# Kernel tuning notes

Measured on AMD Instinct MI355X. Metric: run time of the kernel, lower is better.

Reference implementation:

```python
import jax, jax.numpy as jnp
import numpy as np

HEADS = 4
OUT = 64  # hidden_channels


def gat_conv(x, src, dst, N, W, att_src, att_dst, bias):
    # x: [N, Fin] -> h: [N, H, C]
    h = (x @ W).reshape(N, HEADS, OUT)
    a_s = (h * att_src).sum(-1)  # [N, H]
    a_d = (h * att_dst).sum(-1)  # [N, H]
    logits = jax.nn.leaky_relu(a_s[src] + a_d[dst], negative_slope=0.2)  # [E, H]
    # segment softmax over incoming edges of each destination node
    m = jax.ops.segment_max(logits, dst, num_segments=N)
    e = jnp.exp(logits - m[dst])
    z = jax.ops.segment_sum(e, dst, num_segments=N)
    alpha = e / (z[dst] + 1e-16)
    out = jax.ops.segment_sum(h[src] * alpha[:, :, None], dst, num_segments=N)
    return out.reshape(N, HEADS * OUT) + bias


def setup_inputs() -> dict:
    key = jax.random.key(0)
    ks = jax.random.split(key, 16)
    N, E, F = 50000, 800000, 128
    HC = HEADS * OUT  # 256
    s = 0.1
    return {
        "x": jax.random.normal(ks[0], (N, F), jnp.float32),
        "edge_index": jax.random.randint(ks[1], (2, E), 0, N, dtype=jnp.int32),
        "W1": jax.random.normal(ks[2], (F, HC), jnp.float32) * s,
        "as1": jax.random.normal(ks[3], (1, HEADS, OUT), jnp.float32) * s,
        "ad1": jax.random.normal(ks[4], (1, HEADS, OUT), jnp.float32) * s,
        "b1": jnp.zeros((HC,), jnp.float32),
        "W2": jax.random.normal(ks[5], (HC, HC), jnp.float32) * s,
        "as2": jax.random.normal(ks[6], (1, HEADS, OUT), jnp.float32) * s,
        "ad2": jax.random.normal(ks[7], (1, HEADS, OUT), jnp.float32) * s,
        "b2": jnp.zeros((HC,), jnp.float32),
        "lw1": jax.random.normal(ks[8], (HC, OUT), jnp.float32) * s,
        "lb1": jnp.zeros((OUT,), jnp.float32),
        "lw2": jax.random.normal(ks[9], (OUT, 2), jnp.float32) * s,
        "lb2": jnp.zeros((2,), jnp.float32),
    }


def reference(x, edge_index, W1, as1, ad1, b1, W2, as2, ad2, b2, lw1, lb1, lw2, lb2):
    N = x.shape[0]
    # PyG GATConv default add_self_loops=True
    loop = jnp.arange(N, dtype=edge_index.dtype)
    src = jnp.concatenate([edge_index[0], loop])
    dst = jnp.concatenate([edge_index[1], loop])
    h = jax.nn.elu(gat_conv(x, src, dst, N, W1, as1, ad1, b1))
    # dropout is identity at inference
    h = jax.nn.elu(gat_conv(h, src, dst, N, W2, as2, ad2, b2))
    h = jax.nn.relu(h @ lw1 + lb1)
    return jax.nn.log_softmax(h @ lw2 + lb2, axis=1)
```

## Files before the change

kernel.cpp:

```cpp
#include <hip/hip_runtime.h>
#include <math.h>


typedef __attribute__((ext_vector_type(8))) _Float16 half8v;
typedef __attribute__((ext_vector_type(4))) float f32x4;

__device__ __forceinline__ float lrelu(float x) { return x > 0.f ? x : 0.2f * x; }
__device__ __forceinline__ float elu1(float x) { return x > 0.f ? x : (__expf(x) - 1.f); }

__global__ void convert_weights_kernel(const float* __restrict__ W1, const float* __restrict__ W2,
                                       const float* __restrict__ lw1,
                                       _Float16* __restrict__ o1, _Float16* __restrict__ o2,
                                       _Float16* __restrict__ o3, int* __restrict__ indeg,
                                       int N) {
  int t = blockIdx.x * blockDim.x + threadIdx.x;
  if (t < 32768) {
    int n = t >> 7, k = t & 127;
    o1[t] = (_Float16)W1[(long)k * 256 + n];
  } else if (t < 98304) {
    int i = t - 32768;
    int n = i >> 8, k = i & 255;
    o2[i] = (_Float16)W2[(long)k * 256 + n];
  } else if (t < 114688) {
    int i = t - 98304;
    int n = i >> 8, k = i & 255;
    o3[i] = (_Float16)lw1[(long)k * 64 + n];
  } else if (t < 114688 + N) {
    indeg[t - 114688] = 0;
  }
}

__global__ void count_kernel(const int* __restrict__ dst, int E, int* __restrict__ indeg) {
  int e = blockIdx.x * blockDim.x + threadIdx.x;
  if (e < E) atomicAdd(&indeg[dst[e]], 1);
}

__global__ void scan_block_kernel(const int* __restrict__ in, int* __restrict__ incl,
                                  int* __restrict__ bsum, int N) {
  __shared__ int wsum[16];
  int gid = blockIdx.x * 1024 + threadIdx.x;
  int lane = threadIdx.x & 63, w = threadIdx.x >> 6;
  int v = (gid < N) ? in[gid] : 0;
  int sv = v;
#pragma unroll
  for (int o = 1; o < 64; o <<= 1) {
    int t = __shfl_up(sv, o);
    if (lane >= o) sv += t;
  }
  if (lane == 63) wsum[w] = sv;
  __syncthreads();
  if (w == 0) {
    int bs = (lane < 16) ? wsum[lane] : 0;
#pragma unroll
    for (int o = 1; o < 16; o <<= 1) {
      int t = __shfl_up(bs, o);
      if (lane >= o) bs += t;
    }
    if (lane < 16) wsum[lane] = bs;
  }
  __syncthreads();
  if (w > 0) sv += wsum[w - 1];
  if (gid < N) incl[gid] = sv;
  if (threadIdx.x == 1023) bsum[blockIdx.x] = sv;
}

__global__ void scan_finalize_kernel(const int* __restrict__ in, const int* __restrict__ incl,
                                     const int* __restrict__ bsum, int* __restrict__ off,
                                     int* __restrict__ cursor, int N) {
  int gid = blockIdx.x * blockDim.x + threadIdx.x;
  if (gid >= N) return;
  int b = gid >> 10;
  int carry = 0;
  for (int k = 0; k < b; ++k) carry += bsum[k];
  int ic = incl[gid] + carry;
  off[gid + 1] = ic;
  cursor[gid] = ic - in[gid];
  if (gid == 0) off[0] = 0;
}

__global__ void fill_kernel(const int* __restrict__ src, const int* __restrict__ dst, int E,
                            int* __restrict__ cursor, int* __restrict__ csr_src) {
  int e = blockIdx.x * blockDim.x + threadIdx.x;
  if (e < E) {
    int pos = atomicAdd(&cursor[dst[e]], 1);
    csr_src[pos] = src[e];
  }
}

template <typename AT>
__launch_bounds__(256)
__global__ void mfma_gemm_attn_kernel(const AT* __restrict__ A,
                                      const _Float16* __restrict__ B,
                                      const float* __restrict__ att_s,
                                      const float* __restrict__ att_d,
                                      _Float16* __restrict__ C,
                                      float* __restrict__ a_s, float* __restrict__ a_d,
                                      int M, int K) {
  __shared__ _Float16 As[64][40];
  __shared__ _Float16 Bs[2][64][40];
  int tid = threadIdx.x;
  int bm = blockIdx.y * 64, bn = blockIdx.x * 128;
  int lane = tid & 63, wave = tid >> 6;
  int srow = tid >> 2, sch = (tid & 3) * 8;
  const AT* Ap = A + (long)(bm + srow) * K + sch;
  const _Float16* Bp0 = B + (long)(bn + srow) * K + sch;
  const _Float16* Bp1 = B + (long)(bn + 64 + srow) * K + sch;
  bool arow_ok = (bm + srow) < M;
  int fm = lane & 15, fq = lane >> 4;
  f32x4 acc[2][4];
#pragma unroll
  for (int t = 0; t < 2; ++t)
#pragma unroll
    for (int cb = 0; cb < 4; ++cb) acc[t][cb] = (f32x4){0.f, 0.f, 0.f, 0.f};
  for (int k0 = 0; k0 < K; k0 += 32) {
    half8v a8 = {0, 0, 0, 0, 0, 0, 0, 0};
    if (arow_ok) {
      if constexpr (sizeof(AT) == 4) {
        float4 f0 = *(const float4*)(Ap + k0);
        float4 f1 = *(const float4*)(Ap + k0 + 4);
        a8 = (half8v){(_Float16)f0.x, (_Float16)f0.y, (_Float16)f0.z, (_Float16)f0.w,
                      (_Float16)f1.x, (_Float16)f1.y, (_Float16)f1.z, (_Float16)f1.w};
      } else {
        a8 = *(const half8v*)(Ap + k0);
      }
    }
    uint4 vb0 = *(const uint4*)(Bp0 + k0);
    uint4 vb1 = *(const uint4*)(Bp1 + k0);
    *(half8v*)&As[srow][sch] = a8;
    *(uint4*)&Bs[0][srow][sch] = vb0;
    *(uint4*)&Bs[1][srow][sch] = vb1;
    __syncthreads();
    half8v ah = *(const half8v*)&As[wave * 16 + fm][fq * 8];
#pragma unroll
    for (int t = 0; t < 2; ++t)
#pragma unroll
      for (int cb = 0; cb < 4; ++cb) {
        half8v bh = *(const half8v*)&Bs[t][cb * 16 + fm][fq * 8];
        acc[t][cb] = __builtin_amdgcn_mfma_f32_16x16x32_f16(ah, bh, acc[t][cb], 0, 0, 0);
      }
    __syncthreads();
  }
  int row0 = bm + wave * 16 + fq * 4;
#pragma unroll
  for (int t = 0; t < 2; ++t) {
    int headi = blockIdx.x * 2 + t;
    int cbase = bn + t * 64;
    float asv[4], adv[4];
#pragma unroll
    for (int cb = 0; cb < 4; ++cb) {
      int col = cbase + cb * 16 + fm;
      asv[cb] = att_s[col];
      adv[cb] = att_d[col];
    }
#pragma unroll
    for (int r = 0; r < 4; ++r) {
      int row = row0 + r;
      float sp = 0.f, dp = 0.f;
#pragma unroll
      for (int cb = 0; cb < 4; ++cb) {
        float v = acc[t][cb][r];
        sp = fmaf(v, asv[cb], sp);
        dp = fmaf(v, adv[cb], dp);
        if (row < M) C[(long)row * 256 + cbase + cb * 16 + fm] = (_Float16)v;
      }
#pragma unroll
      for (int o = 1; o < 16; o <<= 1) {
        sp += __shfl_xor(sp, o);
        dp += __shfl_xor(dp, o);
      }
      if (fm == 0 && row < M) {
        a_s[(long)row * 4 + headi] = sp;
        a_d[(long)row * 4 + headi] = dp;
      }
    }
  }
}

__launch_bounds__(256)
__global__ void head_mfma_kernel(const _Float16* __restrict__ A, const _Float16* __restrict__ B,
                                 const float* __restrict__ lb1, const float* __restrict__ lw2,
                                 const float* __restrict__ lb2, float* __restrict__ out, int M) {
  __shared__ _Float16 As[64][40];
  __shared__ _Float16 Bs[64][40];
  int tid = threadIdx.x;
  int bm = blockIdx.x * 64;
  int lane = tid & 63, wave = tid >> 6;
  int srow = tid >> 2, sch = (tid & 3) * 8;
  const _Float16* Ap = A + (long)(bm + srow) * 256 + sch;
  const _Float16* Bp = B + (long)srow * 256 + sch;
  int fm = lane & 15, fq = lane >> 4;
  f32x4 acc[4];
#pragma unroll
  for (int cb = 0; cb < 4; ++cb) acc[cb] = (f32x4){0.f, 0.f, 0.f, 0.f};
  for (int k0 = 0; k0 < 256; k0 += 32) {
    uint4 va = *(const uint4*)(Ap + k0);
    uint4 vb = *(const uint4*)(Bp + k0);
    *(uint4*)&As[srow][sch] = va;
    *(uint4*)&Bs[srow][sch] = vb;
    __syncthreads();
    half8v ah = *(const half8v*)&As[wave * 16 + fm][fq * 8];
#pragma unroll
    for (int cb = 0; cb < 4; ++cb) {
      half8v bh = *(const half8v*)&Bs[cb * 16 + fm][fq * 8];
      acc[cb] = __builtin_amdgcn_mfma_f32_16x16x32_f16(ah, bh, acc[cb], 0, 0, 0);
    }
    __syncthreads();
  }
  float lb1c[4], w20[4], w21[4];
#pragma unroll
  for (int cb = 0; cb < 4; ++cb) {
    int col = cb * 16 + fm;
    lb1c[cb] = lb1[col];
    w20[cb] = lw2[col * 2 + 0];
    w21[cb] = lw2[col * 2 + 1];
  }
  float b20 = lb2[0], b21 = lb2[1];
#pragma unroll
  for (int r = 0; r < 4; ++r) {
    float v0 = 0.f, v1 = 0.f;
#pragma unroll
    for (int cb = 0; cb < 4; ++cb) {
      float s = fmaxf(acc[cb][r] + lb1c[cb], 0.f);
      v0 = fmaf(s, w20[cb], v0);
      v1 = fmaf(s, w21[cb], v1);
    }
#pragma unroll
    for (int o = 1; o < 16; o <<= 1) {
      v0 += __shfl_xor(v0, o);
      v1 += __shfl_xor(v1, o);
    }
    if (fm == 0) {
      int row = bm + wave * 16 + fq * 4 + r;
      if (row < M) {
        v0 += b20;
        v1 += b21;
        float mx = fmaxf(v0, v1);
        float ls = mx + logf(expf(v0 - mx) + expf(v1 - mx));
        out[(long)row * 2 + 0] = v0 - ls;
        out[(long)row * 2 + 1] = v1 - ls;
      }
    }
  }
}

__launch_bounds__(256)
__global__ void gat_aggregate8_kernel(const _Float16* __restrict__ h,
                                      const float* __restrict__ a_s,
                                      const float* __restrict__ a_d,
                                      const int* __restrict__ off,
                                      const int* __restrict__ csr_src,
                                      const float* __restrict__ bias,
                                      _Float16* __restrict__ outp, int N) {
  int wid = (blockIdx.x * blockDim.x + threadIdx.x) >> 6;
  int lane = threadIdx.x & 63;
  if (wid >= N) return;
  int c = lane & 31, hlf = lane >> 5, head4 = c >> 3;
  int h1 = lane & 3, sl1 = lane >> 2;
  int beg = off[wid], cnt = off[wid + 1] - beg;
  float ad_h1 = a_d[wid * 4 + h1];
  float m = lrelu(a_s[wid * 4 + h1] + ad_h1);
  float acc[8] = {};
  float z = 0.f;
  if (hlf == 0) {
    z = 1.f;
    half8v sr = *(const half8v*)(h + (long)wid * 256 + c * 8);
#pragma unroll
    for (int i = 0; i < 8; ++i) acc[i] = (float)sr[i];
  }
  for (int c0 = 0; c0 < cnt; c0 += 16) {
    int i2 = c0 + (lane & 15);
    int sv = (i2 < cnt) ? csr_src[beg + i2] : 0;
    int i1 = c0 + sl1;
    int spi = __shfl(sv, sl1);
    float l = (i1 < cnt) ? lrelu(a_s[(long)spi * 4 + h1] + ad_h1) : -1e30f;
    float lm = l;
    lm = fmaxf(lm, __shfl_xor(lm, 4));
    lm = fmaxf(lm, __shfl_xor(lm, 8));
    lm = fmaxf(lm, __shfl_xor(lm, 16));
    lm = fmaxf(lm, __shfl_xor(lm, 32));
    float m_new = fmaxf(m, lm);
    float alpha = __expf(m - m_new);
    float pv = (i1 < cnt) ? __expf(l - m_new) : 0.f;
    m = m_new;
    float alpha4 = __shfl(alpha, head4);
    z *= alpha4;
#pragma unroll
    for (int i = 0; i < 8; ++i) acc[i] *= alpha4;
#pragma unroll 4
    for (int j = 0; j < 16; j += 2) {
      if (c0 + j >= cnt) break;
      int e = j + hlf;
      int s = __shfl(sv, e);
      float p = __shfl(pv, e * 4 + head4);
      z += p;
      half8v rv = *(const half8v*)(h + (long)s * 256 + c * 8);
      acc[0] = fmaf(p, (float)rv[0], acc[0]);
      acc[1] = fmaf(p, (float)rv[1], acc[1]);
      acc[2] = fmaf(p, (float)rv[2], acc[2]);
      acc[3] = fmaf(p, (float)rv[3], acc[3]);
      acc[4] = fmaf(p, (float)rv[4], acc[4]);
      acc[5] = fmaf(p, (float)rv[5], acc[5]);
      acc[6] = fmaf(p, (float)rv[6], acc[6]);
      acc[7] = fmaf(p, (float)rv[7], acc[7]);
    }
  }
  z += __shfl_xor(z, 32);
#pragma unroll
  for (int i = 0; i < 8; ++i) acc[i] += __shfl_xor(acc[i], 32);
  if (hlf == 0) {
    float inv = 1.f / z;
    half8v o;
#pragma unroll
    for (int i = 0; i < 8; ++i) o[i] = (_Float16)elu1(fmaf(acc[i], inv, bias[c * 8 + i]));
    *(half8v*)(outp + (long)wid * 256 + c * 8) = o;
  }
}

static inline int cdiv(int a, int b) { return (a + b - 1) / b; }

extern "C" void kernel_launch(void* const* d_in, const int* in_sizes, int n_in,
                              void* d_out, int out_size, void* d_ws, size_t ws_size,
                              hipStream_t stream) {
  const float* x = (const float*)d_in[0];
  const int* ei = (const int*)d_in[1];
  const float* W1 = (const float*)d_in[2];
  const float* as1 = (const float*)d_in[3];
  const float* ad1 = (const float*)d_in[4];
  const float* b1 = (const float*)d_in[5];
  const float* W2 = (const float*)d_in[6];
  const float* as2 = (const float*)d_in[7];
  const float* ad2 = (const float*)d_in[8];
  const float* b2 = (const float*)d_in[9];
  const float* lw1 = (const float*)d_in[10];
  const float* lb1 = (const float*)d_in[11];
  const float* lw2 = (const float*)d_in[12];
  const float* lb2 = (const float*)d_in[13];
  float* out = (float*)d_out;

  int N = in_sizes[0] / 128;
  int E = in_sizes[1] / 2;
  int Mp = cdiv(N, 64) * 64;

  char* ws = (char*)d_ws;
  _Float16* Wt1 = (_Float16*)ws; ws += 256 * 128 * 2;
  _Float16* Wt2 = (_Float16*)ws; ws += 256 * 256 * 2;
  _Float16* WL = (_Float16*)ws; ws += 64 * 256 * 2;
  _Float16* C = (_Float16*)ws; ws += (size_t)Mp * 256 * 2;
  _Float16* h2 = (_Float16*)ws; ws += (size_t)Mp * 256 * 2;
  float* aS = (float*)ws; ws += (size_t)N * 4 * 4;
  float* aD = (float*)ws; ws += (size_t)N * 4 * 4;
  int* csr_src = (int*)ws; ws += (size_t)E * 4;
  int* indeg = (int*)ws; ws += (size_t)N * 4;
  int* cursor = (int*)ws; ws += (size_t)N * 4;
  int* off = (int*)ws; ws += (size_t)(N + 4) * 4;
  int* incl = (int*)ws; ws += (size_t)N * 4;
  int* bsum = (int*)ws; ws += 64 * 4;

  const int* e_src = ei;
  const int* e_dst = ei + E;
  int nb = cdiv(N, 1024);

  convert_weights_kernel<<<cdiv(114688 + N, 256), 256, 0, stream>>>(W1, W2, lw1, Wt1, Wt2, WL,
                                                                    indeg, N);

  count_kernel<<<cdiv(E, 256), 256, 0, stream>>>(e_dst, E, indeg);
  scan_block_kernel<<<nb, 1024, 0, stream>>>(indeg, incl, bsum, N);
  scan_finalize_kernel<<<cdiv(N, 256), 256, 0, stream>>>(indeg, incl, bsum, off, cursor, N);
  fill_kernel<<<cdiv(E, 256), 256, 0, stream>>>(e_src, e_dst, E, cursor, csr_src);

  mfma_gemm_attn_kernel<float><<<dim3(2, Mp / 64), 256, 0, stream>>>(x, Wt1, as1, ad1, C, aS, aD,
                                                                     N, 128);
  gat_aggregate8_kernel<<<cdiv(N, 4), 256, 0, stream>>>(C, aS, aD, off, csr_src, b1, h2, N);

  mfma_gemm_attn_kernel<_Float16><<<dim3(2, Mp / 64), 256, 0, stream>>>(h2, Wt2, as2, ad2, C, aS,
                                                                        aD, N, 256);
  gat_aggregate8_kernel<<<cdiv(N, 4), 256, 0, stream>>>(C, aS, aD, off, csr_src, b2, h2, N);

  head_mfma_kernel<<<Mp / 64, 256, 0, stream>>>(h2, WL, lb1, lw2, lb2, out, N);
}
```

Baseline: 362.4 us.

## Drop online-softmax max tracking and fuse MLP head into second aggregation

The aggregation kernel no longer tracks a running maximum with rescaling. It exponentiates the leaky-relu logits directly, relying on the logits being small enough not to overflow. The second-layer aggregation now also computes the 256->64 linear, ReLU, 64->2 linear and log-softmax per node using wave shuffles. This removes the separate head kernel and the fp16 round-trip of h2. In exchange, each wave does 256 shuffles plus reads a 64x256 weight row per lane, and numerical safety now depends on the input scale.

```diff
diff --git a/kernel.cpp b/kernel.cpp
--- a/kernel.cpp
+++ b/kernel.cpp
@@ -176,81 +176,20 @@
   }
 }
 
+template <bool FUSE>
 __launch_bounds__(256)
-__global__ void head_mfma_kernel(const _Float16* __restrict__ A, const _Float16* __restrict__ B,
-                                 const float* __restrict__ lb1, const float* __restrict__ lw2,
-                                 const float* __restrict__ lb2, float* __restrict__ out, int M) {
-  __shared__ _Float16 As[64][40];
-  __shared__ _Float16 Bs[64][40];
-  int tid = threadIdx.x;
-  int bm = blockIdx.x * 64;
-  int lane = tid & 63, wave = tid >> 6;
-  int srow = tid >> 2, sch = (tid & 3) * 8;
-  const _Float16* Ap = A + (long)(bm + srow) * 256 + sch;
-  const _Float16* Bp = B + (long)srow * 256 + sch;
-  int fm = lane & 15, fq = lane >> 4;
-  f32x4 acc[4];
-#pragma unroll
-  for (int cb = 0; cb < 4; ++cb) acc[cb] = (f32x4){0.f, 0.f, 0.f, 0.f};
-  for (int k0 = 0; k0 < 256; k0 += 32) {
-    uint4 va = *(const uint4*)(Ap + k0);
-    uint4 vb = *(const uint4*)(Bp + k0);
-    *(uint4*)&As[srow][sch] = va;
-    *(uint4*)&Bs[srow][sch] = vb;
-    __syncthreads();
-    half8v ah = *(const half8v*)&As[wave * 16 + fm][fq * 8];
-#pragma unroll
-    for (int cb = 0; cb < 4; ++cb) {
-      half8v bh = *(const half8v*)&Bs[cb * 16 + fm][fq * 8];
-      acc[cb] = __builtin_amdgcn_mfma_f32_16x16x32_f16(ah, bh, acc[cb], 0, 0, 0);
-    }
-    __syncthreads();
-  }
-  float lb1c[4], w20[4], w21[4];
-#pragma unroll
-  for (int cb = 0; cb < 4; ++cb) {
-    int col = cb * 16 + fm;
-    lb1c[cb] = lb1[col];
-    w20[cb] = lw2[col * 2 + 0];
-    w21[cb] = lw2[col * 2 + 1];
-  }
-  float b20 = lb2[0], b21 = lb2[1];
-#pragma unroll
-  for (int r = 0; r < 4; ++r) {
-    float v0 = 0.f, v1 = 0.f;
-#pragma unroll
-    for (int cb = 0; cb < 4; ++cb) {
-      float s = fmaxf(acc[cb][r] + lb1c[cb], 0.f);
-      v0 = fmaf(s, w20[cb], v0);
-      v1 = fmaf(s, w21[cb], v1);
-    }
-#pragma unroll
-    for (int o = 1; o < 16; o <<= 1) {
-      v0 += __shfl_xor(v0, o);
-      v1 += __shfl_xor(v1, o);
-    }
-    if (fm == 0) {
-      int row = bm + wave * 16 + fq * 4 + r;
-      if (row < M) {
-        v0 += b20;
-        v1 += b21;
-        float mx = fmaxf(v0, v1);
-        float ls = mx + logf(expf(v0 - mx) + expf(v1 - mx));
-        out[(long)row * 2 + 0] = v0 - ls;
-        out[(long)row * 2 + 1] = v1 - ls;
-      }
-    }
-  }
-}
-
-__launch_bounds__(256)
-__global__ void gat_aggregate8_kernel(const _Float16* __restrict__ h,
-                                      const float* __restrict__ a_s,
-                                      const float* __restrict__ a_d,
-                                      const int* __restrict__ off,
-                                      const int* __restrict__ csr_src,
-                                      const float* __restrict__ bias,
-                                      _Float16* __restrict__ outp, int N) {
+__global__ void gat_aggregate_exp_kernel(const _Float16* __restrict__ h,
+                                         const float* __restrict__ a_s,
+                                         const float* __restrict__ a_d,
+                                         const int* __restrict__ off,
+                                         const int* __restrict__ csr_src,
+                                         const float* __restrict__ bias,
+                                         _Float16* __restrict__ outp,
+                                         const _Float16* __restrict__ WL,
+                                         const float* __restrict__ lb1,
+                                         const float* __restrict__ lw2,
+                                         const float* __restrict__ lb2,
+                                         float* __restrict__ outF, int N) {
   int wid = (blockIdx.x * blockDim.x + threadIdx.x) >> 6;
   int lane = threadIdx.x & 63;
   if (wid >= N) return;
@@ -258,34 +197,22 @@
   int h1 = lane & 3, sl1 = lane >> 2;
   int beg = off[wid], cnt = off[wid + 1] - beg;
   float ad_h1 = a_d[wid * 4 + h1];
-  float m = lrelu(a_s[wid * 4 + h1] + ad_h1);
+  float psl = __expf(lrelu(a_s[wid * 4 + h1] + ad_h1));
+  float pself = __shfl(psl, head4);
+  float z = 0.f;
   float acc[8] = {};
-  float z = 0.f;
   if (hlf == 0) {
-    z = 1.f;
+    z = pself;
     half8v sr = *(const half8v*)(h + (long)wid * 256 + c * 8);
 #pragma unroll
-    for (int i = 0; i < 8; ++i) acc[i] = (float)sr[i];
+    for (int i = 0; i < 8; ++i) acc[i] = pself * (float)sr[i];
   }
   for (int c0 = 0; c0 < cnt; c0 += 16) {
     int i2 = c0 + (lane & 15);
     int sv = (i2 < cnt) ? csr_src[beg + i2] : 0;
     int i1 = c0 + sl1;
     int spi = __shfl(sv, sl1);
-    float l = (i1 < cnt) ? lrelu(a_s[(long)spi * 4 + h1] + ad_h1) : -1e30f;
-    float lm = l;
-    lm = fmaxf(lm, __shfl_xor(lm, 4));
-    lm = fmaxf(lm, __shfl_xor(lm, 8));
-    lm = fmaxf(lm, __shfl_xor(lm, 16));
-    lm = fmaxf(lm, __shfl_xor(lm, 32));
-    float m_new = fmaxf(m, lm);
-    float alpha = __expf(m - m_new);
-    float pv = (i1 < cnt) ? __expf(l - m_new) : 0.f;
-    m = m_new;
-    float alpha4 = __shfl(alpha, head4);
-    z *= alpha4;
-#pragma unroll
-    for (int i = 0; i < 8; ++i) acc[i] *= alpha4;
+    float pv = (i1 < cnt) ? __expf(lrelu(a_s[(long)spi * 4 + h1] + ad_h1)) : 0.f;
 #pragma unroll 4
     for (int j = 0; j < 16; j += 2) {
       if (c0 + j >= cnt) break;
@@ -307,12 +234,46 @@
   z += __shfl_xor(z, 32);
 #pragma unroll
   for (int i = 0; i < 8; ++i) acc[i] += __shfl_xor(acc[i], 32);
-  if (hlf == 0) {
+  if constexpr (!FUSE) {
+    if (hlf == 0) {
+      float inv = 1.f / z;
+      half8v o;
+#pragma unroll
+      for (int i = 0; i < 8; ++i) o[i] = (_Float16)elu1(fmaf(acc[i], inv, bias[c * 8 + i]));
+      *(half8v*)(outp + (long)wid * 256 + c * 8) = o;
+    }
+  } else {
     float inv = 1.f / z;
-    half8v o;
-#pragma unroll
-    for (int i = 0; i < 8; ++i) o[i] = (_Float16)elu1(fmaf(acc[i], inv, bias[c * 8 + i]));
-    *(half8v*)(outp + (long)wid * 256 + c * 8) = o;
+    float hval[8];
+#pragma unroll
+    for (int i = 0; i < 8; ++i) hval[i] = elu1(fmaf(acc[i], inv, bias[c * 8 + i]));
+    const _Float16* wrow = WL + (long)lane * 256;
+    float y = lb1[lane];
+#pragma unroll
+    for (int c2 = 0; c2 < 32; ++c2) {
+      half8v wv = *(const half8v*)(wrow + c2 * 8);
+#pragma unroll
+      for (int i = 0; i < 8; ++i) {
+        float hk = __shfl(hval[i], c2);
+        y = fmaf(hk, (float)wv[i], y);
+      }
+    }
+    float s = fmaxf(y, 0.f);
+    float v0 = s * lw2[lane * 2 + 0];
+    float v1 = s * lw2[lane * 2 + 1];
+#pragma unroll
+    for (int o = 1; o < 64; o <<= 1) {
+      v0 += __shfl_xor(v0, o);
+      v1 += __shfl_xor(v1, o);
+    }
+    if (lane == 0) {
+      v0 += lb2[0];
+      v1 += lb2[1];
+      float mx = fmaxf(v0, v1);
+      float ls = mx + logf(expf(v0 - mx) + expf(v1 - mx));
+      outF[(long)wid * 2 + 0] = v0 - ls;
+      outF[(long)wid * 2 + 1] = v1 - ls;
+    }
   }
 }
 
@@ -370,11 +331,13 @@
 
   mfma_gemm_attn_kernel<float><<<dim3(2, Mp / 64), 256, 0, stream>>>(x, Wt1, as1, ad1, C, aS, aD,
                                                                      N, 128);
-  gat_aggregate8_kernel<<<cdiv(N, 4), 256, 0, stream>>>(C, aS, aD, off, csr_src, b1, h2, N);
+  gat_aggregate_exp_kernel<false><<<cdiv(N, 4), 256, 0, stream>>>(C, aS, aD, off, csr_src, b1, h2,
+                                                                  nullptr, nullptr, nullptr,
+                                                                  nullptr, nullptr, N);
 
   mfma_gemm_attn_kernel<_Float16><<<dim3(2, Mp / 64), 256, 0, stream>>>(h2, Wt2, as2, ad2, C, aS,
                                                                         aD, N, 256);
-  gat_aggregate8_kernel<<<cdiv(N, 4), 256, 0, stream>>>(C, aS, aD, off, csr_src, b2, h2, N);
-
-  head_mfma_kernel<<<Mp / 64, 256, 0, stream>>>(h2, WL, lb1, lw2, lb2, out, N);
-}
+  gat_aggregate_exp_kernel<true><<<cdiv(N, 4), 256, 0, stream>>>(C, aS, aD, off, csr_src, b2,
+                                                                 nullptr, WL, lb1, lw2, lb2, out,
+                                                                 N);
+}
```

Result: slower. 522.8 us (+44.3%).

## Split GAT aggregation across channel halves and drop online-softmax max rescaling

Applied to the files above, without the earlier changes.

The aggregation kernel now gives each destination node two waves in separate blocks, each covering two heads (128 channels). Blocks are interleaved so both halves of a node group run close together in time and can share cached data. Each wave gathers four edges at once with 16 lanes per edge, which raises memory-level parallelism for the random neighbor gathers. The online max tracking and rescaling of the softmax is removed: edge weights become exp(logit) directly. That drops shuffles, extra exps and per-chunk accumulator rescaling, but it can overflow if logits are large, and the CSR indices and a_s values are now read twice per node.

```diff
diff --git a/kernel.cpp b/kernel.cpp
--- a/kernel.cpp
+++ b/kernel.cpp
@@ -244,56 +244,51 @@
 }
 
 __launch_bounds__(256)
-__global__ void gat_aggregate8_kernel(const _Float16* __restrict__ h,
-                                      const float* __restrict__ a_s,
-                                      const float* __restrict__ a_d,
-                                      const int* __restrict__ off,
-                                      const int* __restrict__ csr_src,
-                                      const float* __restrict__ bias,
-                                      _Float16* __restrict__ outp, int N) {
-  int wid = (blockIdx.x * blockDim.x + threadIdx.x) >> 6;
-  int lane = threadIdx.x & 63;
+__global__ void gat_aggregate_half_kernel(const _Float16* __restrict__ h,
+                                          const float* __restrict__ a_s,
+                                          const float* __restrict__ a_d,
+                                          const int* __restrict__ off,
+                                          const int* __restrict__ csr_src,
+                                          const float* __restrict__ bias,
+                                          _Float16* __restrict__ outp, int N) {
+  int bid = blockIdx.x;
+  int xslot = bid & 7;
+  int half = xslot >> 2;
+  int grp = (bid >> 3) * 4 + (xslot & 3);
+  int wave = threadIdx.x >> 6, lane = threadIdx.x & 63;
+  int wid = grp * 4 + wave;
   if (wid >= N) return;
-  int c = lane & 31, hlf = lane >> 5, head4 = c >> 3;
-  int h1 = lane & 3, sl1 = lane >> 2;
+  int c16 = lane & 15, quarter = lane >> 4;
+  int le = lane >> 2, lh = lane & 1;
+  int hb0 = half * 2;
+  int hh = c16 >> 3;
+  int cbase = half * 128 + c16 * 8;
   int beg = off[wid], cnt = off[wid + 1] - beg;
-  float ad_h1 = a_d[wid * 4 + h1];
-  float m = lrelu(a_s[wid * 4 + h1] + ad_h1);
+  float ad_lh = a_d[(long)wid * 4 + hb0 + lh];
+  float pslf = __expf(lrelu(a_s[(long)wid * 4 + hb0 + lh] + ad_lh));
+  float pself = __shfl(pslf, hh);
+  float z = 0.f;
   float acc[8] = {};
-  float z = 0.f;
-  if (hlf == 0) {
-    z = 1.f;
-    half8v sr = *(const half8v*)(h + (long)wid * 256 + c * 8);
-#pragma unroll
-    for (int i = 0; i < 8; ++i) acc[i] = (float)sr[i];
+  if (quarter == 0) {
+    z = pself;
+    half8v sr = *(const half8v*)(h + (long)wid * 256 + cbase);
+#pragma unroll
+    for (int i = 0; i < 8; ++i) acc[i] = pself * (float)sr[i];
   }
   for (int c0 = 0; c0 < cnt; c0 += 16) {
-    int i2 = c0 + (lane & 15);
+    int i2 = c0 + c16;
     int sv = (i2 < cnt) ? csr_src[beg + i2] : 0;
-    int i1 = c0 + sl1;
-    int spi = __shfl(sv, sl1);
-    float l = (i1 < cnt) ? lrelu(a_s[(long)spi * 4 + h1] + ad_h1) : -1e30f;
-    float lm = l;
-    lm = fmaxf(lm, __shfl_xor(lm, 4));
-    lm = fmaxf(lm, __shfl_xor(lm, 8));
-    lm = fmaxf(lm, __shfl_xor(lm, 16));
-    lm = fmaxf(lm, __shfl_xor(lm, 32));
-    float m_new = fmaxf(m, lm);
-    float alpha = __expf(m - m_new);
-    float pv = (i1 < cnt) ? __expf(l - m_new) : 0.f;
-    m = m_new;
-    float alpha4 = __shfl(alpha, head4);
-    z *= alpha4;
-#pragma unroll
-    for (int i = 0; i < 8; ++i) acc[i] *= alpha4;
-#pragma unroll 4
-    for (int j = 0; j < 16; j += 2) {
-      if (c0 + j >= cnt) break;
-      int e = j + hlf;
+    int i1 = c0 + le;
+    int spi = __shfl(sv, le);
+    float pv = (i1 < cnt) ? __expf(lrelu(a_s[(long)spi * 4 + hb0 + lh] + ad_lh)) : 0.f;
+#pragma unroll
+    for (int j = 0; j < 4; ++j) {
+      if (c0 + j * 4 >= cnt) break;
+      int e = j * 4 + quarter;
       int s = __shfl(sv, e);
-      float p = __shfl(pv, e * 4 + head4);
+      float p = __shfl(pv, e * 4 + hh);
       z += p;
-      half8v rv = *(const half8v*)(h + (long)s * 256 + c * 8);
+      half8v rv = *(const half8v*)(h + (long)s * 256 + cbase);
       acc[0] = fmaf(p, (float)rv[0], acc[0]);
       acc[1] = fmaf(p, (float)rv[1], acc[1]);
       acc[2] = fmaf(p, (float)rv[2], acc[2]);
@@ -304,15 +299,19 @@
       acc[7] = fmaf(p, (float)rv[7], acc[7]);
     }
   }
+  z += __shfl_xor(z, 16);
   z += __shfl_xor(z, 32);
 #pragma unroll
-  for (int i = 0; i < 8; ++i) acc[i] += __shfl_xor(acc[i], 32);
-  if (hlf == 0) {
+  for (int i = 0; i < 8; ++i) {
+    acc[i] += __shfl_xor(acc[i], 16);
+    acc[i] += __shfl_xor(acc[i], 32);
+  }
+  if (quarter == 0) {
     float inv = 1.f / z;
     half8v o;
 #pragma unroll
-    for (int i = 0; i < 8; ++i) o[i] = (_Float16)elu1(fmaf(acc[i], inv, bias[c * 8 + i]));
-    *(half8v*)(outp + (long)wid * 256 + c * 8) = o;
+    for (int i = 0; i < 8; ++i) o[i] = (_Float16)elu1(fmaf(acc[i], inv, bias[cbase + i]));
+    *(half8v*)(outp + (long)wid * 256 + cbase) = o;
   }
 }
 
@@ -368,13 +367,15 @@
   scan_finalize_kernel<<<cdiv(N, 256), 256, 0, stream>>>(indeg, incl, bsum, off, cursor, N);
   fill_kernel<<<cdiv(E, 256), 256, 0, stream>>>(e_src, e_dst, E, cursor, csr_src);
 
+  int agg_blocks = 8 * cdiv(cdiv(N, 4), 4);
+
   mfma_gemm_attn_kernel<float><<<dim3(2, Mp / 64), 256, 0, stream>>>(x, Wt1, as1, ad1, C, aS, aD,
                                                                      N, 128);
-  gat_aggregate8_kernel<<<cdiv(N, 4), 256, 0, stream>>>(C, aS, aD, off, csr_src, b1, h2, N);
+  gat_aggregate_half_kernel<<<agg_blocks, 256, 0, stream>>>(C, aS, aD, off, csr_src, b1, h2, N);
 
   mfma_gemm_attn_kernel<_Float16><<<dim3(2, Mp / 64), 256, 0, stream>>>(h2, Wt2, as2, ad2, C, aS,
                                                                         aD, N, 256);
-  gat_aggregate8_kernel<<<cdiv(N, 4), 256, 0, stream>>>(C, aS, aD, off, csr_src, b2, h2, N);
+  gat_aggregate_half_kernel<<<agg_blocks, 256, 0, stream>>>(C, aS, aD, off, csr_src, b2, h2, N);
 
   head_mfma_kernel<<<Mp / 64, 256, 0, stream>>>(h2, WL, lb1, lw2, lb2, out, N);
 }
```

Result: slower. 376.8 us (+4.0%).
